# Kernel tuning notes

Hardware: AMD Instinct MI355X
Metric: run time of the kernel (lower is better)

## Reference

```python
import jax, jax.numpy as jnp
import numpy as np

NUM_OBS_OS = 8
NUM_OBS_TS = 6
HIDDEN = 128
NUM_ACTIONS = 9
B = 32768
N_TS = 32


def setup_inputs() -> dict:
    key = jax.random.key(0)
    ks = jax.random.split(key, 16)
    s_OS = jax.random.normal(ks[0], (B, NUM_OBS_OS), dtype=jnp.float32)
    s_TS = jax.random.normal(ks[1], (B, N_TS, NUM_OBS_TS), dtype=jnp.float32)
    # variable number of valid target ships per row (0..N_TS); trailing slots -> NaN
    lengths = jax.random.randint(ks[2], (B,), 0, N_TS + 1)
    pad = jnp.arange(N_TS)[None, :] >= lengths[:, None]          # [B, N_TS]
    s_TS = jnp.where(pad[:, :, None], jnp.nan, s_TS)
    s = jnp.concatenate([s_OS, s_TS.reshape(B, N_TS * NUM_OBS_TS)], axis=1)

    def lin(k, out_d, in_d):
        bound = 1.0 / np.sqrt(in_d)
        kw, kb = jax.random.split(k)
        W = jax.random.uniform(kw, (out_d, in_d), jnp.float32, -bound, bound)
        b = jax.random.uniform(kb, (out_d,), jnp.float32, -bound, bound)
        return W, b

    W_os, b_os = lin(ks[3], HIDDEN, NUM_OBS_OS)
    bound = 1.0 / np.sqrt(HIDDEN)
    W_ih = jax.random.uniform(ks[4], (4 * HIDDEN, NUM_OBS_TS), jnp.float32, -bound, bound)
    W_hh = jax.random.uniform(ks[5], (4 * HIDDEN, HIDDEN), jnp.float32, -bound, bound)
    b_ih = jax.random.uniform(ks[6], (4 * HIDDEN,), jnp.float32, -bound, bound)
    b_hh = jax.random.uniform(ks[7], (4 * HIDDEN,), jnp.float32, -bound, bound)
    W_ts, b_ts = lin(ks[8], HIDDEN, HIDDEN)
    W_c1, b_c1 = lin(ks[9], HIDDEN, 2 * HIDDEN)
    W_c2, b_c2 = lin(ks[10], NUM_ACTIONS, HIDDEN)
    return {"s": s, "W_os": W_os, "b_os": b_os, "W_ih": W_ih, "W_hh": W_hh,
            "b_ih": b_ih, "b_hh": b_hh, "W_ts": W_ts, "b_ts": b_ts,
            "W_c1": W_c1, "b_c1": b_c1, "W_c2": W_c2, "b_c2": b_c2}


def _lstm(x, W_ih, W_hh, b_ih, b_hh):
    """Single-layer batch-first LSTM; x: [B, T, I] -> outputs [B, T, H]."""
    Bc, T, _ = x.shape
    H = W_hh.shape[1]
    # precompute input projections for all steps: [T, B, 4H]
    xg = jnp.einsum('bti,gi->tbg', x, W_ih) + (b_ih + b_hh)

    def step(carry, xt):
        h, c = carry
        gates = xt + h @ W_hh.T                      # [B, 4H]
        i, f, g, o = jnp.split(gates, 4, axis=-1)    # torch order: i, f, g, o
        i = jax.nn.sigmoid(i)
        f = jax.nn.sigmoid(f)
        g = jnp.tanh(g)
        o = jax.nn.sigmoid(o)
        c = f * c + i * g
        h = o * jnp.tanh(c)
        return (h, c), h

    h0 = jnp.zeros((Bc, H), x.dtype)
    c0 = jnp.zeros((Bc, H), x.dtype)
    _, hs = jax.lax.scan(step, (h0, c0), xg)         # hs: [T, B, H]
    return jnp.transpose(hs, (1, 0, 2))


def reference(s, W_os, b_os, W_ih, W_hh, b_ih, b_hh, W_ts, b_ts, W_c1, b_c1, W_c2, b_c2):
    Bc = s.shape[0]
    s_OS = s[:, :NUM_OBS_OS]
    s_TS = s[:, NUM_OBS_OS:].reshape(Bc, -1, NUM_OBS_TS)          # [B, N_TS, 6]
    valid = jnp.logical_not(jnp.isnan(s_TS[:, :, 0]))             # [B, N_TS]
    n_obs = jnp.sum(valid, axis=1)                                # [B]
    h_idx = jnp.maximum(n_obs, 1) - 1                             # last valid step
    s_TS = jnp.where(jnp.isnan(s_TS), 0.0, s_TS)

    x_OS = jax.nn.relu(s_OS @ W_os.T + b_os)                      # [B, 128]

    out = _lstm(s_TS, W_ih, W_hh, b_ih, b_hh)                     # [B, N_TS, 128]
    x_TS = jnp.take_along_axis(out, h_idx[:, None, None], axis=1)[:, 0]  # [B, 128]
    x_TS = jnp.where((n_obs == 0)[:, None], 0.0, x_TS)
    x_TS = jax.nn.relu(x_TS @ W_ts.T + b_ts)

    x = jnp.concatenate([x_OS, x_TS], axis=1)                     # [B, 256]
    x = jax.nn.relu(x @ W_c1.T + b_c1)
    return x @ W_c2.T + b_c2                                      # [B, num_actions]
```

## Files before the change

### kernel.cpp

```cpp
#include <hip/hip_runtime.h>

#ifndef __has_builtin
#define __has_builtin(x) 0
#endif

#define NOBS_OS 8
#define NOBS_TS 6
#define HID 128
#define NACT 9
#define BTOT 32768
#define NTS 32
#define ROWS 16
#define NTILES 2048
#define PAIRS 1024
#define BLOCK 512
#define PREB 128

#define LEN_OFF 0
#define PERM_OFF BTOT
#define HIST_OFF (2 * BTOT)

typedef __attribute__((ext_vector_type(8))) short short8;
typedef __attribute__((ext_vector_type(4))) float f32x4;

__device__ inline unsigned short f2bf(float x) {
  unsigned int u = __float_as_uint(x);
  u += 0x7FFFu + ((u >> 16) & 1u);
  return (unsigned short)(u >> 16);
}

__device__ inline unsigned pkbf(float a, float b) {
#if __has_builtin(__builtin_amdgcn_cvt_pk_bf16_f32)
  auto v = __builtin_amdgcn_cvt_pk_bf16_f32(a, b);
  unsigned u;
  __builtin_memcpy(&u, &v, sizeof(u));
  return u;
#else
  return ((unsigned)f2bf(b) << 16) | (unsigned)f2bf(a);
#endif
}

__device__ inline float fexp2(float x) {
#if __has_builtin(__builtin_amdgcn_exp2f)
  return __builtin_amdgcn_exp2f(x);
#else
  return exp2f(x);
#endif
}
__device__ inline float frcp_(float x) {
#if __has_builtin(__builtin_amdgcn_rcpf)
  return __builtin_amdgcn_rcpf(x);
#else
  return 1.0f / x;
#endif
}

__device__ inline short8 pack8(f32x4 a, f32x4 b) {
  union { unsigned u[4]; short8 s; } r;
  r.u[0] = pkbf(a[0], a[1]); r.u[1] = pkbf(a[2], a[3]);
  r.u[2] = pkbf(b[0], b[1]); r.u[3] = pkbf(b[2], b[3]);
  return r.s;
}

__device__ inline short8 pack8s(const float* p, float s) {
  union { unsigned u[4]; short8 r; } r;
#pragma unroll
  for (int i = 0; i < 4; ++i) r.u[i] = pkbf(p[2 * i] * s, p[2 * i + 1] * s);
  return r.r;
}

__global__ void count_kernel(const float* __restrict__ s, int* __restrict__ ws) {
  __shared__ int lh[NTS + 1];
  const int tid = threadIdx.x;
  if (tid <= NTS) lh[tid] = 0;
  __syncthreads();
  const int row = blockIdx.x * 256 + tid;
  const float* p = s + (size_t)row * 200 + NOBS_OS;
  int lo = 0, hi = NTS;
  while (lo < hi) {
    const int mid = (lo + hi) >> 1;
    const float v = p[mid * NOBS_TS];
    if (v == v) lo = mid + 1; else hi = mid;
  }
  ws[LEN_OFF + row] = lo;
  atomicAdd(&lh[lo], 1);
  __syncthreads();
  if (tid <= NTS) ws[HIST_OFF + blockIdx.x * (NTS + 1) + tid] = lh[tid];
}

__global__ void scatter_kernel(int* __restrict__ ws) {
  __shared__ int tot[NTS + 1], pre[NTS + 1], gb[NTS + 1], lh[NTS + 1];
  const int tid = threadIdx.x;
  if (tid <= NTS) {
    int t = 0, pr = 0;
    for (int k = 0; k < PREB; ++k) {
      const int h = ws[HIST_OFF + k * (NTS + 1) + tid];
      t += h;
      if (k < (int)blockIdx.x) pr += h;
    }
    tot[tid] = t;
    pre[tid] = pr;
    lh[tid] = 0;
  }
  __syncthreads();
  if (tid == 0) {
    int a = 0;
    for (int b = 0; b <= NTS; ++b) { gb[b] = a; a += tot[b]; }
  }
  __syncthreads();
  const int row = blockIdx.x * 256 + tid;
  const int len = ws[LEN_OFF + row];
  const int r = atomicAdd(&lh[len], 1);
  __syncthreads();
  ws[PERM_OFF + gb[len] + pre[len] + r] = row;
}


#define GX(CN, T)                                                            \
  {                                                                          \
    short8 ax = z8;                                                          \
    if (q == 0) ax = *(const short8*)&x_st[CN][c * 264 + (T) * 8];           \
    _Pragma("unroll") for (int a = 0; a < 4; ++a)                            \
        acc[CN][a] = __builtin_amdgcn_mfma_f32_16x16x32_bf16(                \
            ax, Bh[a][4], biasv[a], 0, 0, 0);                                \
  }

#define GH(CN, T)                                                            \
  {                                                                          \
    const unsigned short* hb = hA[CN][((T) + 1) & 1];                        \
    _Pragma("unroll") for (int kt = 0; kt < 4; ++kt) {                       \
      const short8 ah = *(const short8*)&hb[kt * 512 + L * 8];               \
      _Pragma("unroll") for (int a = 0; a < 4; ++a)                          \
          acc[CN][a] = __builtin_amdgcn_mfma_f32_16x16x32_bf16(              \
              ah, Bh[a][kt], acc[CN][a], 0, 0, 0);                           \
    }                                                                        \
  }

#define ACT(CN, T)                                                           \
  {                                                                          \
    unsigned short* hw = &hA[CN][(T) & 1][pbase];                            \
    float hv[4];                                                             \
    _Pragma("unroll") for (int r = 0; r < 4; ++r) {                          \
      const float ei = fexp2(acc[CN][0][r]);                                 \
      const float ef = fexp2(acc[CN][1][r]);                                 \
      const float eg = fexp2(acc[CN][2][r]);                                 \
      const float eo = fexp2(acc[CN][3][r]);                                 \
      const float rig = frcp_((1.0f + ei) * (1.0f + eg));                    \
      const float rf = frcp_(1.0f + ef);                                     \
      const float cv = cc[CN][r] * rf + (1.0f - eg) * rig;                   \
      cc[CN][r] = cv;                                                        \
      const float ec = fexp2(cv * -2.88539008f);                             \
      const float roc = frcp_((1.0f + eo) * (1.0f + ec));                    \
      hv[r] = (1.0f - ec) * roc;                                             \
    }                                                                        \
    const unsigned p01 = pkbf(hv[0], hv[1]);                                 \
    const unsigned p23 = pkbf(hv[2], hv[3]);                                 \
    hw[0] = (unsigned short)p01;                                             \
    hw[8] = (unsigned short)(p01 >> 16);                                     \
    hw[16] = (unsigned short)p23;                                            \
    hw[24] = (unsigned short)(p23 >> 16);                                    \
    _Pragma("unroll") for (int r = 0; r < 4; ++r) {                          \
      if (((tpck[CN] >> (r * 8)) & 255u) == (unsigned)(T))                   \
        xts[CN][r] = hv[r];                                                  \
    }                                                                        \
  }

__global__ __launch_bounds__(BLOCK, 2) void recdqn_kernel(
    const float* __restrict__ s, const float* __restrict__ W_os,
    const float* __restrict__ b_os, const float* __restrict__ W_ih,
    const float* __restrict__ W_hh, const float* __restrict__ b_ih,
    const float* __restrict__ b_hh, const float* __restrict__ W_ts,
    const float* __restrict__ b_ts, const float* __restrict__ W_c1,
    const float* __restrict__ b_c1, const float* __restrict__ W_c2,
    const float* __restrict__ b_c2, const int* __restrict__ ws,
    float* __restrict__ out) {
  __shared__ unsigned short x_st[2][ROWS * 264];
  __shared__ unsigned short hA[2][2][2048];
  __shared__ unsigned short xtsb[2][2048];
  __shared__ unsigned short xcat[4096];
  __shared__ unsigned short x2b[2048];
  __shared__ int n_lds[2][ROWS];
  __shared__ int rid_s[2][ROWS];
  __shared__ int tmax_sh[2];

  const int tid = threadIdx.x;
  const int L = tid & 63;
  const int w = tid >> 6;
  const int c = L & 15;
  const int q = L >> 4;
  const int j = (w << 4) | c;

  const short8 z8 = {0, 0, 0, 0, 0, 0, 0, 0};

  short8 Bh[4][5];
  f32x4 biasv[4];
#pragma unroll
  for (int a = 0; a < 4; ++a) {
    const float sc = (a == 2) ? -2.88539008f : -1.44269504f;
    const int n = (a << 7) + j;
    const float bb = sc * (b_ih[n] + b_hh[n]);
    f32x4 bv = {bb, bb, bb, bb};
    biasv[a] = bv;
#pragma unroll
    for (int kt = 0; kt < 4; ++kt)
      Bh[a][kt] = pack8s(W_hh + n * HID + kt * 32 + q * 8, sc);
    short8 fx = z8;
    if (q == 0) {
      const float* px = W_ih + n * NOBS_TS;
      union { unsigned u[4]; short8 s; } fu;
      fu.u[0] = pkbf(px[0] * sc, px[1] * sc);
      fu.u[1] = pkbf(px[2] * sc, px[3] * sc);
      fu.u[2] = pkbf(px[4] * sc, px[5] * sc);
      fu.u[3] = 0;
      fx = fu.s;
    }
    Bh[a][4] = fx;
  }

  const int pbase = ((j >> 5) << 9) + (((j >> 3) & 3) << 7) + (q << 5) + (j & 7);

  const int p = (PAIRS - 1) - blockIdx.x;
  if (tid < 32) {
    const int cn = tid >> 4, rr = tid & 15;
    const int row = ws[PERM_OFF + (2 * p + cn) * ROWS + rr];
    rid_s[cn][rr] = row;
    n_lds[cn][rr] = ws[LEN_OFF + row];
  }
  __syncthreads();

#pragma unroll
  for (int it = 0; it < 2; ++it) {
    const int slot = tid + it * 512;
    const int cn = slot >> 9, rt = slot & 511, r = rt >> 5, tq = rt & 31;
    short8 v = z8;
    if (tq < n_lds[cn][r]) {
      const float2* ps =
          (const float2*)(s + (size_t)rid_s[cn][r] * 200 + NOBS_OS + tq * NOBS_TS);
      const float2 A = ps[0], Bv = ps[1], Cv = ps[2];
      union { unsigned u[4]; short8 s; } vu;
      vu.u[0] = pkbf(A.x, A.y);
      vu.u[1] = pkbf(Bv.x, Bv.y);
      vu.u[2] = pkbf(Cv.x, Cv.y);
      vu.u[3] = 0;
      v = vu.s;
    }
    *(short8*)&x_st[cn][r * 264 + tq * 8] = v;
  }
  if (tid == 0) {
#pragma unroll
    for (int cn = 0; cn < 2; ++cn) {
      int mx = 0;
      for (int r = 0; r < ROWS; ++r) mx = max(mx, n_lds[cn][r]);
      tmax_sh[cn] = mx;
    }
  }
  __syncthreads();

  const int tm0 = tmax_sh[0], tm1 = tmax_sh[1];
  unsigned tpck[2];
#pragma unroll
  for (int cn = 0; cn < 2; ++cn) {
    unsigned pk = 0;
#pragma unroll
    for (int b = 0; b < 4; ++b)
      pk |= ((unsigned)((n_lds[cn][q * 4 + b] - 1) & 255)) << (b * 8);
    tpck[cn] = pk;
  }

  float cc[2][4], xts[2][4];
#pragma unroll
  for (int i = 0; i < 4; ++i) {
    cc[0][i] = 0.0f; cc[1][i] = 0.0f;
    xts[0][i] = 0.0f; xts[1][i] = 0.0f;
  }

  f32x4 acc[2][4];
  if (tm1 > 0) {
    if (tm0 > 0) GX(0, 0)
    GX(1, 0)
    if (tm0 > 0) ACT(0, 0)
    ACT(1, 0)
    __syncthreads();
    int t = 1;
    for (; t < tm0; ++t) {
      GX(0, t) GH(0, t)
      GX(1, t) GH(1, t)
      ACT(0, t) ACT(1, t)
      __syncthreads();
    }
    for (; t < tm1; ++t) {
      GX(1, t) GH(1, t)
      ACT(1, t)
      __syncthreads();
    }
  }

#pragma unroll
  for (int cn = 0; cn < 2; ++cn) {
    const unsigned p01 = pkbf(xts[cn][0], xts[cn][1]);
    const unsigned p23 = pkbf(xts[cn][2], xts[cn][3]);
    unsigned short* pw = &xtsb[cn][pbase];
    pw[0] = (unsigned short)p01;
    pw[8] = (unsigned short)(p01 >> 16);
    pw[16] = (unsigned short)p23;
    pw[24] = (unsigned short)(p23 >> 16);
  }
  __syncthreads();

  short8 Fts[4], Fc1[8], Fc2[4], bosf = z8;
#pragma unroll
  for (int kt = 0; kt < 4; ++kt) {
    const f32x4* pp = (const f32x4*)(W_ts + j * HID + kt * 32 + q * 8);
    Fts[kt] = pack8(pp[0], pp[1]);
  }
#pragma unroll
  for (int kt = 0; kt < 8; ++kt) {
    const f32x4* pp = (const f32x4*)(W_c1 + j * 256 + kt * 32 + q * 8);
    Fc1[kt] = pack8(pp[0], pp[1]);
  }
#pragma unroll
  for (int kt = 0; kt < 4; ++kt) Fc2[kt] = z8;
  if (w == 0 && c < NACT) {
#pragma unroll
    for (int kt = 0; kt < 4; ++kt) {
      const f32x4* pp = (const f32x4*)(W_c2 + c * HID + kt * 32 + q * 8);
      Fc2[kt] = pack8(pp[0], pp[1]);
    }
  }
  if (q == 0) {
    const f32x4* pb = (const f32x4*)(W_os + j * NOBS_OS);
    bosf = pack8(pb[0], pb[1]);
  }
  const float bts = b_ts[j], bc1 = b_c1[j], bos = b_os[j];
  const float bc2 = (w == 0 && c < NACT) ? b_c2[c] : 0.0f;

#pragma unroll 1
  for (int cn = 0; cn < 2; ++cn) {
    {
      f32x4 a2 = {bts, bts, bts, bts};
#pragma unroll
      for (int kt = 0; kt < 4; ++kt) {
        const short8 af = *(const short8*)&xtsb[cn][kt * 512 + L * 8];
        a2 = __builtin_amdgcn_mfma_f32_16x16x32_bf16(af, Fts[kt], a2, 0, 0, 0);
      }
      const unsigned p01 = pkbf(fmaxf(a2[0], 0.0f), fmaxf(a2[1], 0.0f));
      const unsigned p23 = pkbf(fmaxf(a2[2], 0.0f), fmaxf(a2[3], 0.0f));
      xcat[2048 + pbase + 0] = (unsigned short)p01;
      xcat[2048 + pbase + 8] = (unsigned short)(p01 >> 16);
      xcat[2048 + pbase + 16] = (unsigned short)p23;
      xcat[2048 + pbase + 24] = (unsigned short)(p23 >> 16);
    }
    {
      short8 aos = z8;
      if (q == 0) {
        const f32x4* pa = (const f32x4*)(s + (size_t)rid_s[cn][c] * 200);
        aos = pack8(pa[0], pa[1]);
      }
      f32x4 a2 = {bos, bos, bos, bos};
      a2 = __builtin_amdgcn_mfma_f32_16x16x32_bf16(aos, bosf, a2, 0, 0, 0);
      const unsigned p01 = pkbf(fmaxf(a2[0], 0.0f), fmaxf(a2[1], 0.0f));
      const unsigned p23 = pkbf(fmaxf(a2[2], 0.0f), fmaxf(a2[3], 0.0f));
      xcat[pbase + 0] = (unsigned short)p01;
      xcat[pbase + 8] = (unsigned short)(p01 >> 16);
      xcat[pbase + 16] = (unsigned short)p23;
      xcat[pbase + 24] = (unsigned short)(p23 >> 16);
    }
    __syncthreads();
    {
      f32x4 a2 = {bc1, bc1, bc1, bc1};
#pragma unroll
      for (int kt = 0; kt < 8; ++kt) {
        const short8 af = *(const short8*)&xcat[kt * 512 + L * 8];
        a2 = __builtin_amdgcn_mfma_f32_16x16x32_bf16(af, Fc1[kt], a2, 0, 0, 0);
      }
      const unsigned p01 = pkbf(fmaxf(a2[0], 0.0f), fmaxf(a2[1], 0.0f));
      const unsigned p23 = pkbf(fmaxf(a2[2], 0.0f), fmaxf(a2[3], 0.0f));
      x2b[pbase + 0] = (unsigned short)p01;
      x2b[pbase + 8] = (unsigned short)(p01 >> 16);
      x2b[pbase + 16] = (unsigned short)p23;
      x2b[pbase + 24] = (unsigned short)(p23 >> 16);
    }
    __syncthreads();
    if (w == 0) {
      f32x4 accf = {bc2, bc2, bc2, bc2};
#pragma unroll
      for (int kt = 0; kt < 4; ++kt) {
        const short8 af = *(const short8*)&x2b[kt * 512 + L * 8];
        accf = __builtin_amdgcn_mfma_f32_16x16x32_bf16(af, Fc2[kt], accf, 0, 0, 0);
      }
      if (c < NACT) {
#pragma unroll
        for (int r = 0; r < 4; ++r)
          out[(size_t)rid_s[cn][q * 4 + r] * NACT + c] = accf[r];
      }
    }
    __syncthreads();
  }
}

extern "C" void kernel_launch(void* const* d_in, const int* in_sizes, int n_in,
                              void* d_out, int out_size, void* d_ws, size_t ws_size,
                              hipStream_t stream) {
  (void)in_sizes; (void)n_in; (void)out_size; (void)ws_size;
  const float* s    = (const float*)d_in[0];
  const float* W_os = (const float*)d_in[1];
  const float* b_os = (const float*)d_in[2];
  const float* W_ih = (const float*)d_in[3];
  const float* W_hh = (const float*)d_in[4];
  const float* b_ih = (const float*)d_in[5];
  const float* b_hh = (const float*)d_in[6];
  const float* W_ts = (const float*)d_in[7];
  const float* b_ts = (const float*)d_in[8];
  const float* W_c1 = (const float*)d_in[9];
  const float* b_c1 = (const float*)d_in[10];
  const float* W_c2 = (const float*)d_in[11];
  const float* b_c2 = (const float*)d_in[12];
  int* ws = (int*)d_ws;
  float* outp = (float*)d_out;

  count_kernel<<<PREB, 256, 0, stream>>>(s, ws);
  scatter_kernel<<<PREB, 256, 0, stream>>>(ws);
  recdqn_kernel<<<PAIRS, BLOCK, 0, stream>>>(
      s, W_os, b_os, W_ih, W_hh, b_ih, b_hh, W_ts, b_ts, W_c1, b_c1, W_c2,
      b_c2, ws, outp);
}
```

Baseline: 278.6 us.

## Split the two row-tiles across separate 512-thread wave groups in a 1024-thread block

Each block now runs 1024 threads, with each half (g) owning one 16-row tile instead of every wave interleaving both tiles. This halves per-thread accumulator and cell-state registers. The W_ih fragment moves to LDS with the bias folded in through a constant-1 input column, and the last-valid hidden state is written straight to LDS in bf16 rather than held in registers. The cost is that both groups share barriers for max(tmax) steps, the occupancy hint of 2 blocks per CU is dropped, and each step now reads W_ih fragments from LDS.

```diff
diff --git a/kernel.cpp b/kernel.cpp
--- a/kernel.cpp
+++ b/kernel.cpp
@@ -13,7 +13,7 @@
 #define ROWS 16
 #define NTILES 2048
 #define PAIRS 1024
-#define BLOCK 512
+#define BLOCK 1024
 #define PREB 128
 
 #define LEN_OFF 0
@@ -116,56 +116,61 @@
 }
 
 
-#define GX(CN, T)                                                            \
+#define GX(T)                                                                \
   {                                                                          \
     short8 ax = z8;                                                          \
-    if (q == 0) ax = *(const short8*)&x_st[CN][c * 264 + (T) * 8];           \
-    _Pragma("unroll") for (int a = 0; a < 4; ++a)                            \
-        acc[CN][a] = __builtin_amdgcn_mfma_f32_16x16x32_bf16(                \
-            ax, Bh[a][4], biasv[a], 0, 0, 0);                                \
-  }
-
-#define GH(CN, T)                                                            \
+    if (q == 0) ax = *(const short8*)&xstg[c * 264 + (T) * 8];               \
+    _Pragma("unroll") for (int a = 0; a < 4; ++a) {                          \
+      const short8 wf = *(const short8*)&wihf[(a * 128 + j) * 8];            \
+      acc[a] = __builtin_amdgcn_mfma_f32_16x16x32_bf16(ax, wf, z4, 0, 0, 0); \
+    }                                                                        \
+  }
+
+#define GH(T)                                                                \
   {                                                                          \
-    const unsigned short* hb = hA[CN][((T) + 1) & 1];                        \
+    const unsigned short* hb = hAg + ((((T) + 1) & 1) << 11);                \
     _Pragma("unroll") for (int kt = 0; kt < 4; ++kt) {                       \
       const short8 ah = *(const short8*)&hb[kt * 512 + L * 8];               \
       _Pragma("unroll") for (int a = 0; a < 4; ++a)                          \
-          acc[CN][a] = __builtin_amdgcn_mfma_f32_16x16x32_bf16(              \
-              ah, Bh[a][kt], acc[CN][a], 0, 0, 0);                           \
+          acc[a] = __builtin_amdgcn_mfma_f32_16x16x32_bf16(                  \
+              ah, Bh[a][kt], acc[a], 0, 0, 0);                               \
     }                                                                        \
   }
 
-#define ACT(CN, T)                                                           \
+#define ACT(T)                                                               \
   {                                                                          \
-    unsigned short* hw = &hA[CN][(T) & 1][pbase];                            \
+    unsigned short* hw = hAg + (((T) & 1) << 11) + pbase;                    \
     float hv[4];                                                             \
     _Pragma("unroll") for (int r = 0; r < 4; ++r) {                          \
-      const float ei = fexp2(acc[CN][0][r]);                                 \
-      const float ef = fexp2(acc[CN][1][r]);                                 \
-      const float eg = fexp2(acc[CN][2][r]);                                 \
-      const float eo = fexp2(acc[CN][3][r]);                                 \
+      const float ei = fexp2(acc[0][r]);                                     \
+      const float ef = fexp2(acc[1][r]);                                     \
+      const float eg = fexp2(acc[2][r]);                                     \
+      const float eo = fexp2(acc[3][r]);                                     \
       const float rig = frcp_((1.0f + ei) * (1.0f + eg));                    \
       const float rf = frcp_(1.0f + ef);                                     \
-      const float cv = cc[CN][r] * rf + (1.0f - eg) * rig;                   \
-      cc[CN][r] = cv;                                                        \
+      const float cv = cc[r] * rf + (1.0f - eg) * rig;                       \
+      cc[r] = cv;                                                            \
       const float ec = fexp2(cv * -2.88539008f);                             \
       const float roc = frcp_((1.0f + eo) * (1.0f + ec));                    \
       hv[r] = (1.0f - ec) * roc;                                             \
     }                                                                        \
     const unsigned p01 = pkbf(hv[0], hv[1]);                                 \
     const unsigned p23 = pkbf(hv[2], hv[3]);                                 \
-    hw[0] = (unsigned short)p01;                                             \
-    hw[8] = (unsigned short)(p01 >> 16);                                     \
-    hw[16] = (unsigned short)p23;                                            \
-    hw[24] = (unsigned short)(p23 >> 16);                                    \
-    _Pragma("unroll") for (int r = 0; r < 4; ++r) {                          \
-      if (((tpck[CN] >> (r * 8)) & 255u) == (unsigned)(T))                   \
-        xts[CN][r] = hv[r];                                                  \
-    }                                                                        \
-  }
-
-__global__ __launch_bounds__(BLOCK, 2) void recdqn_kernel(
+    const unsigned short hb16_0 = (unsigned short)p01;                       \
+    const unsigned short hb16_1 = (unsigned short)(p01 >> 16);               \
+    const unsigned short hb16_2 = (unsigned short)p23;                       \
+    const unsigned short hb16_3 = (unsigned short)(p23 >> 16);               \
+    hw[0] = hb16_0;                                                          \
+    hw[8] = hb16_1;                                                          \
+    hw[16] = hb16_2;                                                         \
+    hw[24] = hb16_3;                                                         \
+    if (((tpck >> 0) & 255u) == (unsigned)(T)) xtsbg[pbase + 0] = hb16_0;    \
+    if (((tpck >> 8) & 255u) == (unsigned)(T)) xtsbg[pbase + 8] = hb16_1;    \
+    if (((tpck >> 16) & 255u) == (unsigned)(T)) xtsbg[pbase + 16] = hb16_2;  \
+    if (((tpck >> 24) & 255u) == (unsigned)(T)) xtsbg[pbase + 24] = hb16_3;  \
+  }
+
+__global__ __launch_bounds__(BLOCK) void recdqn_kernel(
     const float* __restrict__ s, const float* __restrict__ W_os,
     const float* __restrict__ b_os, const float* __restrict__ W_ih,
     const float* __restrict__ W_hh, const float* __restrict__ b_ih,
@@ -177,8 +182,9 @@
   __shared__ unsigned short x_st[2][ROWS * 264];
   __shared__ unsigned short hA[2][2][2048];
   __shared__ unsigned short xtsb[2][2048];
-  __shared__ unsigned short xcat[4096];
-  __shared__ unsigned short x2b[2048];
+  __shared__ unsigned short wihf[4 * 128 * 8];
+  __shared__ unsigned short xcat[2][4096];
+  __shared__ unsigned short x2b[2][2048];
   __shared__ int n_lds[2][ROWS];
   __shared__ int rid_s[2][ROWS];
   __shared__ int tmax_sh[2];
@@ -186,35 +192,23 @@
   const int tid = threadIdx.x;
   const int L = tid & 63;
   const int w = tid >> 6;
+  const int g = w >> 3;
+  const int ww = w & 7;
   const int c = L & 15;
   const int q = L >> 4;
-  const int j = (w << 4) | c;
+  const int j = (ww << 4) | c;
 
   const short8 z8 = {0, 0, 0, 0, 0, 0, 0, 0};
-
-  short8 Bh[4][5];
-  f32x4 biasv[4];
+  const f32x4 z4 = {0.0f, 0.0f, 0.0f, 0.0f};
+
+  short8 Bh[4][4];
 #pragma unroll
   for (int a = 0; a < 4; ++a) {
     const float sc = (a == 2) ? -2.88539008f : -1.44269504f;
     const int n = (a << 7) + j;
-    const float bb = sc * (b_ih[n] + b_hh[n]);
-    f32x4 bv = {bb, bb, bb, bb};
-    biasv[a] = bv;
 #pragma unroll
     for (int kt = 0; kt < 4; ++kt)
       Bh[a][kt] = pack8s(W_hh + n * HID + kt * 32 + q * 8, sc);
-    short8 fx = z8;
-    if (q == 0) {
-      const float* px = W_ih + n * NOBS_TS;
-      union { unsigned u[4]; short8 s; } fu;
-      fu.u[0] = pkbf(px[0] * sc, px[1] * sc);
-      fu.u[1] = pkbf(px[2] * sc, px[3] * sc);
-      fu.u[2] = pkbf(px[4] * sc, px[5] * sc);
-      fu.u[3] = 0;
-      fx = fu.s;
-    }
-    Bh[a][4] = fx;
   }
 
   const int pbase = ((j >> 5) << 9) + (((j >> 3) & 3) << 7) + (q << 5) + (j & 7);
@@ -226,12 +220,22 @@
     rid_s[cn][rr] = row;
     n_lds[cn][rr] = ws[LEN_OFF + row];
   }
-  __syncthreads();
-
-#pragma unroll
-  for (int it = 0; it < 2; ++it) {
-    const int slot = tid + it * 512;
-    const int cn = slot >> 9, rt = slot & 511, r = rt >> 5, tq = rt & 31;
+  if (tid < 512) {
+    const int a = tid >> 7, jj = tid & 127, n = (a << 7) + jj;
+    const float sc = (a == 2) ? -2.88539008f : -1.44269504f;
+    const float* px = W_ih + n * NOBS_TS;
+    union { unsigned u[4]; short8 s; } fu;
+    fu.u[0] = pkbf(px[0] * sc, px[1] * sc);
+    fu.u[1] = pkbf(px[2] * sc, px[3] * sc);
+    fu.u[2] = pkbf(px[4] * sc, px[5] * sc);
+    fu.u[3] = pkbf(sc * (b_ih[n] + b_hh[n]), 0.0f);
+    *(short8*)&wihf[tid * 8] = fu.s;
+    *(short8*)&((unsigned short*)xtsb)[tid * 8] = z8;
+  }
+  __syncthreads();
+
+  {
+    const int cn = tid >> 9, rt = tid & 511, r = rt >> 5, tq = rt & 31;
     short8 v = z8;
     if (tq < n_lds[cn][r]) {
       const float2* ps =
@@ -241,7 +245,7 @@
       vu.u[0] = pkbf(A.x, A.y);
       vu.u[1] = pkbf(Bv.x, Bv.y);
       vu.u[2] = pkbf(Cv.x, Cv.y);
-      vu.u[3] = 0;
+      vu.u[3] = pkbf(1.0f, 0.0f);
       v = vu.s;
     }
     *(short8*)&x_st[cn][r * 264 + tq * 8] = v;
@@ -256,56 +260,27 @@
   }
   __syncthreads();
 
-  const int tm0 = tmax_sh[0], tm1 = tmax_sh[1];
-  unsigned tpck[2];
-#pragma unroll
-  for (int cn = 0; cn < 2; ++cn) {
-    unsigned pk = 0;
-#pragma unroll
-    for (int b = 0; b < 4; ++b)
-      pk |= ((unsigned)((n_lds[cn][q * 4 + b] - 1) & 255)) << (b * 8);
-    tpck[cn] = pk;
-  }
-
-  float cc[2][4], xts[2][4];
-#pragma unroll
-  for (int i = 0; i < 4; ++i) {
-    cc[0][i] = 0.0f; cc[1][i] = 0.0f;
-    xts[0][i] = 0.0f; xts[1][i] = 0.0f;
-  }
-
-  f32x4 acc[2][4];
+  const int tm1 = tmax_sh[1];
+  const int tmg = tmax_sh[g];
+  unsigned tpck = 0;
+#pragma unroll
+  for (int b = 0; b < 4; ++b)
+    tpck |= ((unsigned)((n_lds[g][q * 4 + b] - 1) & 255)) << (b * 8);
+
+  float cc[4] = {0.0f, 0.0f, 0.0f, 0.0f};
+  const unsigned short* xstg = &x_st[g][0];
+  unsigned short* hAg = &hA[g][0][0];
+  unsigned short* xtsbg = &xtsb[g][0];
+
+  f32x4 acc[4];
   if (tm1 > 0) {
-    if (tm0 > 0) GX(0, 0)
-    GX(1, 0)
-    if (tm0 > 0) ACT(0, 0)
-    ACT(1, 0)
+    if (tmg > 0) { GX(0) ACT(0) }
     __syncthreads();
-    int t = 1;
-    for (; t < tm0; ++t) {
-      GX(0, t) GH(0, t)
-      GX(1, t) GH(1, t)
-      ACT(0, t) ACT(1, t)
+    for (int t = 1; t < tm1; ++t) {
+      if (t < tmg) { GX(t) GH(t) ACT(t) }
       __syncthreads();
     }
-    for (; t < tm1; ++t) {
-      GX(1, t) GH(1, t)
-      ACT(1, t)
-      __syncthreads();
-    }
-  }
-
-#pragma unroll
-  for (int cn = 0; cn < 2; ++cn) {
-    const unsigned p01 = pkbf(xts[cn][0], xts[cn][1]);
-    const unsigned p23 = pkbf(xts[cn][2], xts[cn][3]);
-    unsigned short* pw = &xtsb[cn][pbase];
-    pw[0] = (unsigned short)p01;
-    pw[8] = (unsigned short)(p01 >> 16);
-    pw[16] = (unsigned short)p23;
-    pw[24] = (unsigned short)(p23 >> 16);
-  }
-  __syncthreads();
+  }
 
   short8 Fts[4], Fc1[8], Fc2[4], bosf = z8;
 #pragma unroll
@@ -320,7 +295,7 @@
   }
 #pragma unroll
   for (int kt = 0; kt < 4; ++kt) Fc2[kt] = z8;
-  if (w == 0 && c < NACT) {
+  if (ww == 0 && c < NACT) {
 #pragma unroll
     for (int kt = 0; kt < 4; ++kt) {
       const f32x4* pp = (const f32x4*)(W_c2 + c * HID + kt * 32 + q * 8);
@@ -332,69 +307,65 @@
     bosf = pack8(pb[0], pb[1]);
   }
   const float bts = b_ts[j], bc1 = b_c1[j], bos = b_os[j];
-  const float bc2 = (w == 0 && c < NACT) ? b_c2[c] : 0.0f;
-
-#pragma unroll 1
-  for (int cn = 0; cn < 2; ++cn) {
-    {
-      f32x4 a2 = {bts, bts, bts, bts};
-#pragma unroll
-      for (int kt = 0; kt < 4; ++kt) {
-        const short8 af = *(const short8*)&xtsb[cn][kt * 512 + L * 8];
-        a2 = __builtin_amdgcn_mfma_f32_16x16x32_bf16(af, Fts[kt], a2, 0, 0, 0);
-      }
-      const unsigned p01 = pkbf(fmaxf(a2[0], 0.0f), fmaxf(a2[1], 0.0f));
-      const unsigned p23 = pkbf(fmaxf(a2[2], 0.0f), fmaxf(a2[3], 0.0f));
-      xcat[2048 + pbase + 0] = (unsigned short)p01;
-      xcat[2048 + pbase + 8] = (unsigned short)(p01 >> 16);
-      xcat[2048 + pbase + 16] = (unsigned short)p23;
-      xcat[2048 + pbase + 24] = (unsigned short)(p23 >> 16);
-    }
-    {
-      short8 aos = z8;
-      if (q == 0) {
-        const f32x4* pa = (const f32x4*)(s + (size_t)rid_s[cn][c] * 200);
-        aos = pack8(pa[0], pa[1]);
-      }
-      f32x4 a2 = {bos, bos, bos, bos};
-      a2 = __builtin_amdgcn_mfma_f32_16x16x32_bf16(aos, bosf, a2, 0, 0, 0);
-      const unsigned p01 = pkbf(fmaxf(a2[0], 0.0f), fmaxf(a2[1], 0.0f));
-      const unsigned p23 = pkbf(fmaxf(a2[2], 0.0f), fmaxf(a2[3], 0.0f));
-      xcat[pbase + 0] = (unsigned short)p01;
-      xcat[pbase + 8] = (unsigned short)(p01 >> 16);
-      xcat[pbase + 16] = (unsigned short)p23;
-      xcat[pbase + 24] = (unsigned short)(p23 >> 16);
-    }
-    __syncthreads();
-    {
-      f32x4 a2 = {bc1, bc1, bc1, bc1};
-#pragma unroll
-      for (int kt = 0; kt < 8; ++kt) {
-        const short8 af = *(const short8*)&xcat[kt * 512 + L * 8];
-        a2 = __builtin_amdgcn_mfma_f32_16x16x32_bf16(af, Fc1[kt], a2, 0, 0, 0);
-      }
-      const unsigned p01 = pkbf(fmaxf(a2[0], 0.0f), fmaxf(a2[1], 0.0f));
-      const unsigned p23 = pkbf(fmaxf(a2[2], 0.0f), fmaxf(a2[3], 0.0f));
-      x2b[pbase + 0] = (unsigned short)p01;
-      x2b[pbase + 8] = (unsigned short)(p01 >> 16);
-      x2b[pbase + 16] = (unsigned short)p23;
-      x2b[pbase + 24] = (unsigned short)(p23 >> 16);
-    }
-    __syncthreads();
-    if (w == 0) {
-      f32x4 accf = {bc2, bc2, bc2, bc2};
-#pragma unroll
-      for (int kt = 0; kt < 4; ++kt) {
-        const short8 af = *(const short8*)&x2b[kt * 512 + L * 8];
-        accf = __builtin_amdgcn_mfma_f32_16x16x32_bf16(af, Fc2[kt], accf, 0, 0, 0);
-      }
-      if (c < NACT) {
-#pragma unroll
-        for (int r = 0; r < 4; ++r)
-          out[(size_t)rid_s[cn][q * 4 + r] * NACT + c] = accf[r];
-      }
-    }
-    __syncthreads();
+  const float bc2 = (ww == 0 && c < NACT) ? b_c2[c] : 0.0f;
+
+  {
+    f32x4 a2 = {bts, bts, bts, bts};
+#pragma unroll
+    for (int kt = 0; kt < 4; ++kt) {
+      const short8 af = *(const short8*)&xtsbg[kt * 512 + L * 8];
+      a2 = __builtin_amdgcn_mfma_f32_16x16x32_bf16(af, Fts[kt], a2, 0, 0, 0);
+    }
+    const unsigned p01 = pkbf(fmaxf(a2[0], 0.0f), fmaxf(a2[1], 0.0f));
+    const unsigned p23 = pkbf(fmaxf(a2[2], 0.0f), fmaxf(a2[3], 0.0f));
+    xcat[g][2048 + pbase + 0] = (unsigned short)p01;
+    xcat[g][2048 + pbase + 8] = (unsigned short)(p01 >> 16);
+    xcat[g][2048 + pbase + 16] = (unsigned short)p23;
+    xcat[g][2048 + pbase + 24] = (unsigned short)(p23 >> 16);
+  }
+  {
+    short8 aos = z8;
+    if (q == 0) {
+      const f32x4* pa = (const f32x4*)(s + (size_t)rid_s[g][c] * 200);
+      aos = pack8(pa[0], pa[1]);
+    }
+    f32x4 a2 = {bos, bos, bos, bos};
+    a2 = __builtin_amdgcn_mfma_f32_16x16x32_bf16(aos, bosf, a2, 0, 0, 0);
+    const unsigned p01 = pkbf(fmaxf(a2[0], 0.0f), fmaxf(a2[1], 0.0f));
+    const unsigned p23 = pkbf(fmaxf(a2[2], 0.0f), fmaxf(a2[3], 0.0f));
+    xcat[g][pbase + 0] = (unsigned short)p01;
+    xcat[g][pbase + 8] = (unsigned short)(p01 >> 16);
+    xcat[g][pbase + 16] = (unsigned short)p23;
+    xcat[g][pbase + 24] = (unsigned short)(p23 >> 16);
+  }
+  __syncthreads();
+  {
+    f32x4 a2 = {bc1, bc1, bc1, bc1};
+#pragma unroll
+    for (int kt = 0; kt < 8; ++kt) {
+      const short8 af = *(const short8*)&xcat[g][kt * 512 + L * 8];
+      a2 = __builtin_amdgcn_mfma_f32_16x16x32_bf16(af, Fc1[kt], a2, 0, 0, 0);
+    }
+    const unsigned p01 = pkbf(fmaxf(a2[0], 0.0f), fmaxf(a2[1], 0.0f));
+    const unsigned p23 = pkbf(fmaxf(a2[2], 0.0f), fmaxf(a2[3], 0.0f));
+    x2b[g][pbase + 0] = (unsigned short)p01;
+    x2b[g][pbase + 8] = (unsigned short)(p01 >> 16);
+    x2b[g][pbase + 16] = (unsigned short)p23;
+    x2b[g][pbase + 24] = (unsigned short)(p23 >> 16);
+  }
+  __syncthreads();
+  if (ww == 0) {
+    f32x4 accf = {bc2, bc2, bc2, bc2};
+#pragma unroll
+    for (int kt = 0; kt < 4; ++kt) {
+      const short8 af = *(const short8*)&x2b[g][kt * 512 + L * 8];
+      accf = __builtin_amdgcn_mfma_f32_16x16x32_bf16(af, Fc2[kt], accf, 0, 0, 0);
+    }
+    if (c < NACT) {
+#pragma unroll
+      for (int r = 0; r < 4; ++r)
+        out[(size_t)rid_s[g][q * 4 + r] * NACT + c] = accf[r];
+    }
   }
 }
 
```

Result: slower. 372.8 us (+33.8%).
